# Performance work log

Hardware: AMD Instinct MI355X
Metric: run time of the kernel (lower is better)

Reference implementation:

```python
import jax, jax.numpy as jnp
import numpy as np

B, C, N, D, E = 2048, 3, 1568, 16, 8  # batch, classes, input caps, out dim, in dim
T_ROUTING = 3


def squash(t, axis=-1):
    sq_norm = jnp.sum(t * t, axis=axis, keepdims=True)
    return (sq_norm / (1.0 + sq_norm)) * t / jnp.sqrt(sq_norm)


def setup_inputs() -> dict:
    key = jax.random.key(0)
    k1, k2 = jax.random.split(key)
    x = jax.random.normal(k1, (B, N, E), dtype=jnp.float32)
    W = 0.001 * jax.random.normal(k2, (1, C, N, D, E), dtype=jnp.float32)
    return {"x": x, "W": W}


def reference(x, W):
    # u_hat = W @ x[:, None, :, :, None]  -> (B, C, N, D) (trailing 1-dim dropped)
    u = jnp.einsum('ocnde,bne->bcnd', W, x)
    b = jnp.zeros((B, C, N), dtype=u.dtype)  # routing logits
    v = None
    for _ in range(T_ROUTING):
        c = jax.nn.softmax(b, axis=1)               # coupling coeffs over classes
        s = jnp.einsum('bcnd,bcn->bcd', u, c)       # weighted sum over input caps
        v = squash(s)                               # (B, C, D)
        b = b + jnp.einsum('bcd,bcnd->bcn', v, u)   # agreement update
    return v
```

## Files before the change

### kernel.cpp

```cpp
#include <hip/hip_runtime.h>
#include <hip/hip_fp16.h>

#define BB 2048
#define NN 1568
#define CD 48

__device__ __forceinline__ unsigned packh2(float a, float b) {
    __half2 h = __floats2half2_rn(a, b);
    unsigned r; __builtin_memcpy(&r, &h, 4); return r;
}
__device__ __forceinline__ float2 uph2(unsigned v) {
    __half2 h; __builtin_memcpy(&h, &v, 4); return __half22float2(h);
}

__global__ __launch_bounds__(256, 3)
void k1_u(const float* __restrict__ x, const float* __restrict__ W,
          __half* __restrict__ u)
{
    __shared__ float wlds[16 * 384];
    const int t  = threadIdx.x;
    const int bl = t & 31;
    const int h  = (t >> 5) & 1;
    const int ns = t >> 6;
    const int bg = blockIdx.x & 63;
    const int g  = blockIdx.x >> 6;
    const int b  = bg * 32 + bl;
    const int n0 = g * 16;

    float xr[32];
#pragma unroll
    for (int i = 0; i < 4; ++i) {
        const float* xp = x + ((size_t)b * NN + n0 + ns * 4 + i) * 8;
        const float4 a = __ldg((const float4*)xp);
        const float4 c = __ldg((const float4*)(xp + 4));
        xr[i*8+0]=a.x; xr[i*8+1]=a.y; xr[i*8+2]=a.z; xr[i*8+3]=a.w;
        xr[i*8+4]=c.x; xr[i*8+5]=c.y; xr[i*8+6]=c.z; xr[i*8+7]=c.w;
    }

#pragma unroll
    for (int k = 0; k < 6; ++k) {
        const int q = t + k * 256;
        const int c = q >> 9;
        const int j = (q >> 5) & 15;
        const int f = q & 31;
        const float4 v = *(const float4*)(W + (((size_t)(c * NN + n0 + j)) << 7) + (f << 2));
        *(float4*)(wlds + j * 384 + c * 128 + (f << 2)) = v;
    }
    __syncthreads();

#pragma unroll
    for (int i = 0; i < 4; ++i) {
        const int nr = ns * 4 + i;
        const int n  = n0 + nr;
        const float x0 = xr[i*8+0], x1 = xr[i*8+1], x2 = xr[i*8+2], x3 = xr[i*8+3];
        const float x4 = xr[i*8+4], x5 = xr[i*8+5], x6 = xr[i*8+6], x7 = xr[i*8+7];
        __half* dst = u + ((size_t)b * NN + n) * CD + h * 8;

#pragma unroll
        for (int c = 0; c < 3; ++c) {
            const float* wc = wlds + nr * 384 + c * 128 + h * 64;
            uint4 pk;
#pragma unroll
            for (int pp = 0; pp < 4; ++pp) {
                const float4 w0 = *(const float4*)(wc + 16 * pp);
                const float4 w1 = *(const float4*)(wc + 16 * pp + 4);
                const float4 w2 = *(const float4*)(wc + 16 * pp + 8);
                const float4 w3 = *(const float4*)(wc + 16 * pp + 12);
                const float a0 = w0.x*x0 + w0.y*x1 + w0.z*x2 + w0.w*x3
                               + w1.x*x4 + w1.y*x5 + w1.z*x6 + w1.w*x7;
                const float a1 = w2.x*x0 + w2.y*x1 + w2.z*x2 + w2.w*x3
                               + w3.x*x4 + w3.y*x5 + w3.z*x6 + w3.w*x7;
                const unsigned pv = packh2(a0, a1);
                if (pp == 0) pk.x = pv; else if (pp == 1) pk.y = pv;
                else if (pp == 2) pk.z = pv; else pk.w = pv;
            }
            *(uint4*)(dst + c * 16) = pk;
        }
    }
}

__global__ __launch_bounds__(256, 3)
void k2_route(const __half* __restrict__ u, float* __restrict__ out)
{
    __shared__ float red[4][CD];
    __shared__ float vsh[CD];

    const int t = threadIdx.x;
    const int w = t >> 6;
    const int b = blockIdx.x;
    const __half* ub = u + (size_t)b * NN * CD;

    float acc[CD];

#pragma unroll
    for (int i = 0; i < CD; ++i) acc[i] = 0.f;
    for (int n = t; n < NN; n += 256) {
        const uint4* p = (const uint4*)(ub + (size_t)n * CD);
        const uint4 r0 = p[0], r1 = p[1], r2 = p[2], r3 = p[3], r4 = p[4], r5 = p[5];
        const unsigned rr[24] = { r0.x,r0.y,r0.z,r0.w, r1.x,r1.y,r1.z,r1.w,
                                  r2.x,r2.y,r2.z,r2.w, r3.x,r3.y,r3.z,r3.w,
                                  r4.x,r4.y,r4.z,r4.w, r5.x,r5.y,r5.z,r5.w };
#pragma unroll
        for (int j = 0; j < 24; ++j) {
            const float2 f = uph2(rr[j]);
            acc[2*j] += f.x; acc[2*j+1] += f.y;
        }
    }
#pragma unroll
    for (int i = 0; i < CD; ++i) {
        float v = acc[i];
        v += __shfl_xor(v, 1); v += __shfl_xor(v, 2); v += __shfl_xor(v, 4);
        v += __shfl_xor(v, 8); v += __shfl_xor(v, 16); v += __shfl_xor(v, 32);
        acc[i] = v;
    }
    if ((t & 63) == 0) { for (int i = 0; i < CD; ++i) red[w][i] = acc[i]; }
    __syncthreads();
    if (t < CD) {
        float s = (red[0][t] + red[1][t] + red[2][t] + red[3][t]) * (1.0f / 3.0f);
        float q = s * s;
        q += __shfl_xor(q, 1); q += __shfl_xor(q, 2); q += __shfl_xor(q, 4); q += __shfl_xor(q, 8);
        vsh[t] = s * sqrtf(q) / (1.f + q);
    }
    __syncthreads();

#pragma unroll 1
    for (int pass = 1; pass <= 2; ++pass) {
        float wv[CD];
#pragma unroll
        for (int i = 0; i < CD; ++i) wv[i] = vsh[i];
#pragma unroll
        for (int i = 0; i < CD; ++i) acc[i] = 0.f;

        for (int n = t; n < NN; n += 256) {
            const uint4* p = (const uint4*)(ub + (size_t)n * CD);
            const uint4 r0 = p[0], r1 = p[1], r2 = p[2], r3 = p[3], r4 = p[4], r5 = p[5];
            const unsigned rr[24] = { r0.x,r0.y,r0.z,r0.w, r1.x,r1.y,r1.z,r1.w,
                                      r2.x,r2.y,r2.z,r2.w, r3.x,r3.y,r3.z,r3.w,
                                      r4.x,r4.y,r4.z,r4.w, r5.x,r5.y,r5.z,r5.w };
            float l0 = 0.f, l1 = 0.f, l2 = 0.f;
#pragma unroll
            for (int j = 0; j < 8; ++j) {
                const float2 f0 = uph2(rr[j]);
                const float2 f1 = uph2(rr[8 + j]);
                const float2 f2 = uph2(rr[16 + j]);
                l0 += wv[2*j]      * f0.x + wv[2*j+1]      * f0.y;
                l1 += wv[16+2*j]   * f1.x + wv[16+2*j+1]   * f1.y;
                l2 += wv[32+2*j]   * f2.x + wv[32+2*j+1]   * f2.y;
            }
            const float e0 = __expf(l0), e1 = __expf(l1), e2 = __expf(l2);
            const float inv = 1.f / (e0 + e1 + e2);
            const float c0 = e0 * inv, c1 = e1 * inv, c2 = e2 * inv;
#pragma unroll
            for (int j = 0; j < 8; ++j) {
                const float2 f0 = uph2(rr[j]);
                const float2 f1 = uph2(rr[8 + j]);
                const float2 f2 = uph2(rr[16 + j]);
                acc[2*j]      += c0 * f0.x;  acc[2*j+1]      += c0 * f0.y;
                acc[16+2*j]   += c1 * f1.x;  acc[16+2*j+1]   += c1 * f1.y;
                acc[32+2*j]   += c2 * f2.x;  acc[32+2*j+1]   += c2 * f2.y;
            }
        }
#pragma unroll
        for (int i = 0; i < CD; ++i) {
            float v = acc[i];
            v += __shfl_xor(v, 1); v += __shfl_xor(v, 2); v += __shfl_xor(v, 4);
            v += __shfl_xor(v, 8); v += __shfl_xor(v, 16); v += __shfl_xor(v, 32);
            acc[i] = v;
        }
        if ((t & 63) == 0) { for (int i = 0; i < CD; ++i) red[w][i] = acc[i]; }
        __syncthreads();
        if (t < CD) {
            const float s = red[0][t] + red[1][t] + red[2][t] + red[3][t];
            float q = s * s;
            q += __shfl_xor(q, 1); q += __shfl_xor(q, 2); q += __shfl_xor(q, 4); q += __shfl_xor(q, 8);
            const float v = s * sqrtf(q) / (1.f + q);
            if (pass == 1) vsh[t] = wv[t] + v;
            else           out[b * CD + t] = v;
        }
        __syncthreads();
    }
}

extern "C" void kernel_launch(void* const* d_in, const int* in_sizes, int n_in,
                              void* d_out, int out_size, void* d_ws, size_t ws_size,
                              hipStream_t stream) {
    (void)in_sizes; (void)n_in; (void)out_size;
    const float* x = (const float*)d_in[0];
    const float* W = (const float*)d_in[1];
    const size_t u_bytes = (size_t)BB * NN * CD * sizeof(__half);
    if (ws_size < u_bytes) return;
    __half* u = (__half*)d_ws;

    hipLaunchKernelGGL(k1_u,     dim3(98 * 64), dim3(256), 0, stream, x, W, u);
    hipLaunchKernelGGL(k2_route, dim3(BB),      dim3(256), 0, stream, u, (float*)d_out);
}
```

Baseline: 435.5 us.

## Drop LDS staging of W in u-projection kernel and read W directly per wavefront

```diff
diff --git a/kernel.cpp b/kernel.cpp
--- a/kernel.cpp
+++ b/kernel.cpp
@@ -13,63 +13,40 @@
     __half2 h; __builtin_memcpy(&h, &v, 4); return __half22float2(h);
 }
 
-__global__ __launch_bounds__(256, 3)
+__global__ __launch_bounds__(64, 6)
 void k1_u(const float* __restrict__ x, const float* __restrict__ W,
           __half* __restrict__ u)
 {
-    __shared__ float wlds[16 * 384];
-    const int t  = threadIdx.x;
-    const int bl = t & 31;
-    const int h  = (t >> 5) & 1;
-    const int ns = t >> 6;
+    const int l  = threadIdx.x;
+    const int bl = l & 31;
+    const int h  = l >> 5;
     const int bg = blockIdx.x & 63;
     const int g  = blockIdx.x >> 6;
     const int b  = bg * 32 + bl;
-    const int n0 = g * 16;
+    const int n0 = g * 8;
 
-    float xr[32];
-#pragma unroll
-    for (int i = 0; i < 4; ++i) {
-        const float* xp = x + ((size_t)b * NN + n0 + ns * 4 + i) * 8;
-        const float4 a = __ldg((const float4*)xp);
-        const float4 c = __ldg((const float4*)(xp + 4));
-        xr[i*8+0]=a.x; xr[i*8+1]=a.y; xr[i*8+2]=a.z; xr[i*8+3]=a.w;
-        xr[i*8+4]=c.x; xr[i*8+5]=c.y; xr[i*8+6]=c.z; xr[i*8+7]=c.w;
-    }
-
-#pragma unroll
-    for (int k = 0; k < 6; ++k) {
-        const int q = t + k * 256;
-        const int c = q >> 9;
-        const int j = (q >> 5) & 15;
-        const int f = q & 31;
-        const float4 v = *(const float4*)(W + (((size_t)(c * NN + n0 + j)) << 7) + (f << 2));
-        *(float4*)(wlds + j * 384 + c * 128 + (f << 2)) = v;
-    }
-    __syncthreads();
-
-#pragma unroll
-    for (int i = 0; i < 4; ++i) {
-        const int nr = ns * 4 + i;
-        const int n  = n0 + nr;
-        const float x0 = xr[i*8+0], x1 = xr[i*8+1], x2 = xr[i*8+2], x3 = xr[i*8+3];
-        const float x4 = xr[i*8+4], x5 = xr[i*8+5], x6 = xr[i*8+6], x7 = xr[i*8+7];
+#pragma unroll 2
+    for (int i = 0; i < 8; ++i) {
+        const int n = n0 + i;
+        const float* xp = x + ((size_t)b * NN + n) * 8;
+        const float4 xa = __ldg((const float4*)xp);
+        const float4 xb = __ldg((const float4*)(xp + 4));
         __half* dst = u + ((size_t)b * NN + n) * CD + h * 8;
 
 #pragma unroll
         for (int c = 0; c < 3; ++c) {
-            const float* wc = wlds + nr * 384 + c * 128 + h * 64;
+            const float* wc = W + ((size_t)(c * NN + n)) * 128 + h * 64;
             uint4 pk;
 #pragma unroll
             for (int pp = 0; pp < 4; ++pp) {
-                const float4 w0 = *(const float4*)(wc + 16 * pp);
-                const float4 w1 = *(const float4*)(wc + 16 * pp + 4);
-                const float4 w2 = *(const float4*)(wc + 16 * pp + 8);
-                const float4 w3 = *(const float4*)(wc + 16 * pp + 12);
-                const float a0 = w0.x*x0 + w0.y*x1 + w0.z*x2 + w0.w*x3
-                               + w1.x*x4 + w1.y*x5 + w1.z*x6 + w1.w*x7;
-                const float a1 = w2.x*x0 + w2.y*x1 + w2.z*x2 + w2.w*x3
-                               + w3.x*x4 + w3.y*x5 + w3.z*x6 + w3.w*x7;
+                const float4 w0 = __ldg((const float4*)(wc + 16 * pp));
+                const float4 w1 = __ldg((const float4*)(wc + 16 * pp + 4));
+                const float4 w2 = __ldg((const float4*)(wc + 16 * pp + 8));
+                const float4 w3 = __ldg((const float4*)(wc + 16 * pp + 12));
+                const float a0 = w0.x*xa.x + w0.y*xa.y + w0.z*xa.z + w0.w*xa.w
+                               + w1.x*xb.x + w1.y*xb.y + w1.z*xb.z + w1.w*xb.w;
+                const float a1 = w2.x*xa.x + w2.y*xa.y + w2.z*xa.z + w2.w*xa.w
+                               + w3.x*xb.x + w3.y*xb.y + w3.z*xb.z + w3.w*xb.w;
                 const unsigned pv = packh2(a0, a1);
                 if (pp == 0) pk.x = pv; else if (pp == 1) pk.y = pv;
                 else if (pp == 2) pk.z = pv; else pk.w = pv;
@@ -191,6 +168,6 @@
     if (ws_size < u_bytes) return;
     __half* u = (__half*)d_ws;
 
-    hipLaunchKernelGGL(k1_u,     dim3(98 * 64), dim3(256), 0, stream, x, W, u);
-    hipLaunchKernelGGL(k2_route, dim3(BB),      dim3(256), 0, stream, u, (float*)d_out);
+    hipLaunchKernelGGL(k1_u,     dim3(196 * 64), dim3(64),  0, stream, x, W, u);
+    hipLaunchKernelGGL(k2_route, dim3(BB),       dim3(256), 0, stream, u, (float*)d_out);
 }
```

Result: slower. 586.3 us (+34.6%).

## Fuse first routing pass sum into u-computation kernel via atomics

Applied to the files above, without the earlier changes.

```diff
diff --git a/kernel.cpp b/kernel.cpp
--- a/kernel.cpp
+++ b/kernel.cpp
@@ -15,27 +15,21 @@
 
 __global__ __launch_bounds__(256, 3)
 void k1_u(const float* __restrict__ x, const float* __restrict__ W,
-          __half* __restrict__ u)
+          __half* __restrict__ u, float* __restrict__ s1g)
 {
     __shared__ float wlds[16 * 384];
+    __shared__ float s1l[32 * 49];
     const int t  = threadIdx.x;
-    const int bl = t & 31;
-    const int h  = (t >> 5) & 1;
-    const int ns = t >> 6;
+    const int bl = t & 15;
+    const int h  = (t >> 4) & 1;
+    const int ns = t >> 5;
     const int bg = blockIdx.x & 63;
     const int g  = blockIdx.x >> 6;
-    const int b  = bg * 32 + bl;
     const int n0 = g * 16;
-
-    float xr[32];
-#pragma unroll
-    for (int i = 0; i < 4; ++i) {
-        const float* xp = x + ((size_t)b * NN + n0 + ns * 4 + i) * 8;
-        const float4 a = __ldg((const float4*)xp);
-        const float4 c = __ldg((const float4*)(xp + 4));
-        xr[i*8+0]=a.x; xr[i*8+1]=a.y; xr[i*8+2]=a.z; xr[i*8+3]=a.w;
-        xr[i*8+4]=c.x; xr[i*8+5]=c.y; xr[i*8+6]=c.z; xr[i*8+7]=c.w;
-    }
+    const int b1 = bg * 32 + bl;
+    const int b2 = b1 + 16;
+
+    for (int k = t; k < 32 * 49; k += 256) s1l[k] = 0.f;
 
 #pragma unroll
     for (int k = 0; k < 6; ++k) {
@@ -48,39 +42,87 @@
     }
     __syncthreads();
 
-#pragma unroll
-    for (int i = 0; i < 4; ++i) {
-        const int nr = ns * 4 + i;
+    float acc[48];
+#pragma unroll
+    for (int i = 0; i < 48; ++i) acc[i] = 0.f;
+
+#pragma unroll
+    for (int i = 0; i < 2; ++i) {
+        const int nr = ns * 2 + i;
         const int n  = n0 + nr;
-        const float x0 = xr[i*8+0], x1 = xr[i*8+1], x2 = xr[i*8+2], x3 = xr[i*8+3];
-        const float x4 = xr[i*8+4], x5 = xr[i*8+5], x6 = xr[i*8+6], x7 = xr[i*8+7];
-        __half* dst = u + ((size_t)b * NN + n) * CD + h * 8;
+        const float* xp1 = x + ((size_t)b1 * NN + n) * 8;
+        const float* xp2 = x + ((size_t)b2 * NN + n) * 8;
+        const float4 xa1 = __ldg((const float4*)xp1), xb1 = __ldg((const float4*)(xp1 + 4));
+        const float4 xa2 = __ldg((const float4*)xp2), xb2 = __ldg((const float4*)(xp2 + 4));
+        __half* d1 = u + ((size_t)b1 * NN + n) * CD + h * 8;
+        __half* d2 = u + ((size_t)b2 * NN + n) * CD + h * 8;
 
 #pragma unroll
         for (int c = 0; c < 3; ++c) {
             const float* wc = wlds + nr * 384 + c * 128 + h * 64;
-            uint4 pk;
+            uint4 p1, p2;
 #pragma unroll
             for (int pp = 0; pp < 4; ++pp) {
                 const float4 w0 = *(const float4*)(wc + 16 * pp);
                 const float4 w1 = *(const float4*)(wc + 16 * pp + 4);
                 const float4 w2 = *(const float4*)(wc + 16 * pp + 8);
                 const float4 w3 = *(const float4*)(wc + 16 * pp + 12);
-                const float a0 = w0.x*x0 + w0.y*x1 + w0.z*x2 + w0.w*x3
-                               + w1.x*x4 + w1.y*x5 + w1.z*x6 + w1.w*x7;
-                const float a1 = w2.x*x0 + w2.y*x1 + w2.z*x2 + w2.w*x3
-                               + w3.x*x4 + w3.y*x5 + w3.z*x6 + w3.w*x7;
-                const unsigned pv = packh2(a0, a1);
-                if (pp == 0) pk.x = pv; else if (pp == 1) pk.y = pv;
-                else if (pp == 2) pk.z = pv; else pk.w = pv;
+                const float a0 = w0.x*xa1.x + w0.y*xa1.y + w0.z*xa1.z + w0.w*xa1.w
+                               + w1.x*xb1.x + w1.y*xb1.y + w1.z*xb1.z + w1.w*xb1.w;
+                const float a1 = w2.x*xa1.x + w2.y*xa1.y + w2.z*xa1.z + w2.w*xa1.w
+                               + w3.x*xb1.x + w3.y*xb1.y + w3.z*xb1.z + w3.w*xb1.w;
+                const float q0 = w0.x*xa2.x + w0.y*xa2.y + w0.z*xa2.z + w0.w*xa2.w
+                               + w1.x*xb2.x + w1.y*xb2.y + w1.z*xb2.z + w1.w*xb2.w;
+                const float q1 = w2.x*xa2.x + w2.y*xa2.y + w2.z*xa2.z + w2.w*xa2.w
+                               + w3.x*xb2.x + w3.y*xb2.y + w3.z*xb2.z + w3.w*xb2.w;
+                acc[c*8 + 2*pp]          += a0;
+                acc[c*8 + 2*pp + 1]      += a1;
+                acc[24 + c*8 + 2*pp]     += q0;
+                acc[24 + c*8 + 2*pp + 1] += q1;
+                const unsigned v1p = packh2(a0, a1);
+                const unsigned v2p = packh2(q0, q1);
+                if (pp == 0) { p1.x = v1p; p2.x = v2p; }
+                else if (pp == 1) { p1.y = v1p; p2.y = v2p; }
+                else if (pp == 2) { p1.z = v1p; p2.z = v2p; }
+                else { p1.w = v1p; p2.w = v2p; }
             }
-            *(uint4*)(dst + c * 16) = pk;
-        }
-    }
-}
-
-__global__ __launch_bounds__(256, 3)
-void k2_route(const __half* __restrict__ u, float* __restrict__ out)
+            *(uint4*)(d1 + c * 16) = p1;
+            *(uint4*)(d2 + c * 16) = p2;
+        }
+    }
+
+#pragma unroll
+    for (int c = 0; c < 3; ++c) {
+#pragma unroll
+        for (int dd = 0; dd < 8; ++dd) {
+            atomicAdd(&s1l[bl * 49 + c * 16 + h * 8 + dd], acc[c*8 + dd]);
+            atomicAdd(&s1l[(bl + 16) * 49 + c * 16 + h * 8 + dd], acc[24 + c*8 + dd]);
+        }
+    }
+    __syncthreads();
+    for (int k = t; k < 1536; k += 256) {
+        const int j  = k / 48;
+        const int cd = k - j * 48;
+        atomicAdd(&s1g[(bg * 32 + j) * CD + cd], s1l[j * 49 + cd]);
+    }
+}
+
+__global__ __launch_bounds__(256, 4)
+void k_squash(float* __restrict__ s1)
+{
+    const int t = blockIdx.x * 256 + threadIdx.x;
+    const float2 a = *(const float2*)(s1 + 2 * t);
+    const float s0 = a.x * (1.0f / 3.0f), s1v = a.y * (1.0f / 3.0f);
+    float q = s0 * s0 + s1v * s1v;
+    q += __shfl_xor(q, 1); q += __shfl_xor(q, 2); q += __shfl_xor(q, 4);
+    const float f = sqrtf(q) / (1.f + q);
+    float2 o; o.x = s0 * f; o.y = s1v * f;
+    *(float2*)(s1 + 2 * t) = o;
+}
+
+__global__ __launch_bounds__(256, 4)
+void k2_route(const __half* __restrict__ u, const float* __restrict__ v1,
+              float* __restrict__ out)
 {
     __shared__ float red[4][CD];
     __shared__ float vsh[CD];
@@ -90,38 +132,10 @@
     const int b = blockIdx.x;
     const __half* ub = u + (size_t)b * NN * CD;
 
+    if (t < CD) vsh[t] = v1[b * CD + t];
+    __syncthreads();
+
     float acc[CD];
-
-#pragma unroll
-    for (int i = 0; i < CD; ++i) acc[i] = 0.f;
-    for (int n = t; n < NN; n += 256) {
-        const uint4* p = (const uint4*)(ub + (size_t)n * CD);
-        const uint4 r0 = p[0], r1 = p[1], r2 = p[2], r3 = p[3], r4 = p[4], r5 = p[5];
-        const unsigned rr[24] = { r0.x,r0.y,r0.z,r0.w, r1.x,r1.y,r1.z,r1.w,
-                                  r2.x,r2.y,r2.z,r2.w, r3.x,r3.y,r3.z,r3.w,
-                                  r4.x,r4.y,r4.z,r4.w, r5.x,r5.y,r5.z,r5.w };
-#pragma unroll
-        for (int j = 0; j < 24; ++j) {
-            const float2 f = uph2(rr[j]);
-            acc[2*j] += f.x; acc[2*j+1] += f.y;
-        }
-    }
-#pragma unroll
-    for (int i = 0; i < CD; ++i) {
-        float v = acc[i];
-        v += __shfl_xor(v, 1); v += __shfl_xor(v, 2); v += __shfl_xor(v, 4);
-        v += __shfl_xor(v, 8); v += __shfl_xor(v, 16); v += __shfl_xor(v, 32);
-        acc[i] = v;
-    }
-    if ((t & 63) == 0) { for (int i = 0; i < CD; ++i) red[w][i] = acc[i]; }
-    __syncthreads();
-    if (t < CD) {
-        float s = (red[0][t] + red[1][t] + red[2][t] + red[3][t]) * (1.0f / 3.0f);
-        float q = s * s;
-        q += __shfl_xor(q, 1); q += __shfl_xor(q, 2); q += __shfl_xor(q, 4); q += __shfl_xor(q, 8);
-        vsh[t] = s * sqrtf(q) / (1.f + q);
-    }
-    __syncthreads();
 
 #pragma unroll 1
     for (int pass = 1; pass <= 2; ++pass) {
@@ -187,10 +201,14 @@
     (void)in_sizes; (void)n_in; (void)out_size;
     const float* x = (const float*)d_in[0];
     const float* W = (const float*)d_in[1];
-    const size_t u_bytes = (size_t)BB * NN * CD * sizeof(__half);
-    if (ws_size < u_bytes) return;
-    __half* u = (__half*)d_ws;
-
-    hipLaunchKernelGGL(k1_u,     dim3(98 * 64), dim3(256), 0, stream, x, W, u);
-    hipLaunchKernelGGL(k2_route, dim3(BB),      dim3(256), 0, stream, u, (float*)d_out);
-}
+    const size_t u_bytes  = (size_t)BB * NN * CD * sizeof(__half);
+    const size_t s1_bytes = (size_t)BB * CD * sizeof(float);
+    if (ws_size < u_bytes + s1_bytes) return;
+    __half* u  = (__half*)d_ws;
+    float*  s1 = (float*)((char*)d_ws + u_bytes);
+
+    hipMemsetAsync(s1, 0, s1_bytes, stream);
+    hipLaunchKernelGGL(k1_u,     dim3(98 * 64), dim3(256), 0, stream, x, W, u, s1);
+    hipLaunchKernelGGL(k_squash, dim3((BB * CD / 2) / 256), dim3(256), 0, stream, s1);
+    hipLaunchKernelGGL(k2_route, dim3(BB), dim3(256), 0, stream, u, s1, (float*)d_out);
+}
```

Result: slower. 845.0 us (+94.0%).
